# Kernel tuning notes

Hardware: AMD Instinct MI355X
Metric: run time of the kernel (lower is better)

Reference implementation:

```python
import jax, jax.numpy as jnp
import numpy as np

N = 50000      # nodes
E = 800000     # edges (before self-loops)
G = 128        # graphs in batch
IN = 128       # in_channels
HID = 32       # hidden_channels (per head)
HEADS = 4
OUT = 64       # out_channels
SLOPE = 0.2    # PyG GATConv default negative_slope


def setup_inputs() -> dict:
    key = jax.random.key(0)
    ks = jax.random.split(key, 24)
    s = 0.1
    inp = {
        'x': jax.random.normal(ks[0], (N, IN), jnp.float32),
        'edge_index': jax.random.randint(ks[1], (2, E), 0, N, dtype=jnp.int32),
        'batch': jnp.sort(jax.random.randint(ks[2], (N,), 0, G, dtype=jnp.int32)),
        # conv1: IN -> HEADS*HID, concat
        'W1': jax.random.normal(ks[3], (IN, HEADS * HID), jnp.float32) * s,
        'a1s': jax.random.normal(ks[4], (HEADS, HID), jnp.float32) * s,
        'a1d': jax.random.normal(ks[5], (HEADS, HID), jnp.float32) * s,
        'b1': jnp.zeros((HEADS * HID,), jnp.float32),
        # conv2: HEADS*HID -> HEADS*HID, concat
        'W2': jax.random.normal(ks[6], (HEADS * HID, HEADS * HID), jnp.float32) * s,
        'a2s': jax.random.normal(ks[7], (HEADS, HID), jnp.float32) * s,
        'a2d': jax.random.normal(ks[8], (HEADS, HID), jnp.float32) * s,
        'b2': jnp.zeros((HEADS * HID,), jnp.float32),
        # conv3
        'W3': jax.random.normal(ks[9], (HEADS * HID, HEADS * HID), jnp.float32) * s,
        'a3s': jax.random.normal(ks[10], (HEADS, HID), jnp.float32) * s,
        'a3d': jax.random.normal(ks[11], (HEADS, HID), jnp.float32) * s,
        'b3': jnp.zeros((HEADS * HID,), jnp.float32),
        # conv4: heads=1, concat=False -> HID
        'W4': jax.random.normal(ks[12], (HEADS * HID, 1 * HID), jnp.float32) * s,
        'a4s': jax.random.normal(ks[13], (1, HID), jnp.float32) * s,
        'a4d': jax.random.normal(ks[14], (1, HID), jnp.float32) * s,
        'b4': jnp.zeros((HID,), jnp.float32),
        # fc: HID -> OUT
        'fcW': jax.random.normal(ks[15], (HID, OUT), jnp.float32) * s,
        'fcb': jnp.zeros((OUT,), jnp.float32),
    }
    return inp


def gat_conv(x, src, dst, W, a_src, a_dst, bias, heads, ch, concat):
    # x: [N, F_in]; src/dst: [E'] with self-loops (PyG add_self_loops=True)
    h = (x @ W).reshape(N, heads, ch)                       # [N, H, C]
    alpha_s = jnp.einsum('nhc,hc->nh', h, a_src)            # [N, H]
    alpha_d = jnp.einsum('nhc,hc->nh', h, a_dst)
    e = jax.nn.leaky_relu(alpha_s[src] + alpha_d[dst], SLOPE)  # [E', H]
    # segment softmax over edges grouped by destination node
    e_max = jax.ops.segment_max(e, dst, num_segments=N)
    e = jnp.exp(e - e_max[dst])
    denom = jax.ops.segment_sum(e, dst, num_segments=N)
    alpha = e / (denom[dst] + 1e-16)                        # [E', H]
    msg = h[src] * alpha[:, :, None]                        # [E', H, C]
    out = jax.ops.segment_sum(msg, dst, num_segments=N)     # [N, H, C]
    out = out.reshape(N, heads * ch) if concat else out.mean(axis=1)
    return out + bias


def reference(x, edge_index, batch, W1, a1s, a1d, b1, W2, a2s, a2d, b2,
              W3, a3s, a3d, b3, W4, a4s, a4d, b4, fcW, fcb):
    loop = jnp.arange(N, dtype=edge_index.dtype)
    src = jnp.concatenate([edge_index[0], loop])            # add self-loops once
    dst = jnp.concatenate([edge_index[1], loop])
    h = jax.nn.elu(gat_conv(x, src, dst, W1, a1s, a1d, b1, HEADS, HID, True))
    h = jax.nn.elu(gat_conv(h, src, dst, W2, a2s, a2d, b2, HEADS, HID, True))
    h = jax.nn.elu(gat_conv(h, src, dst, W3, a3s, a3d, b3, HEADS, HID, True))
    h = jax.nn.elu(gat_conv(h, src, dst, W4, a4s, a4d, b4, 1, HID, False))
    # global mean pool over graphs
    counts = jax.ops.segment_sum(jnp.ones((N,), h.dtype), batch, num_segments=G)
    pooled = jax.ops.segment_sum(h, batch, num_segments=G) / jnp.maximum(counts, 1.0)[:, None]
    # dropout p=0.5 is identity at inference
    return pooled @ fcW + fcb                               # [G, OUT]
```

## Files before the change

kernel.cpp:

```cpp
#include <hip/hip_runtime.h>


constexpr int NN     = 50000;
constexpr int NNPAD  = 50048;
constexpr int EE     = 800000;
constexpr int ETOT   = EE + NN;
constexpr int GG     = 128;
constexpr int HIDC   = 32;
constexpr int OUTC   = 64;

constexpr int NRANGE = (NN + 127) / 128;
constexpr int EPB    = 4096;
constexpr int NBLK   = (EE + EPB - 1) / EPB;
constexpr int RCAP   = 2688;

typedef short  bf16x8 __attribute__((ext_vector_type(8)));
typedef float  f32x4  __attribute__((ext_vector_type(4)));

static __device__ __forceinline__ unsigned short f2bf(float f) {
    unsigned int u = __float_as_uint(f);
    unsigned int r = (u + 0x7fffu + ((u >> 16) & 1u)) >> 16;
    return (unsigned short)r;
}
static __device__ __forceinline__ float bflo(unsigned int v) {
    return __uint_as_float(v << 16);
}
static __device__ __forceinline__ float bfhi(unsigned int v) {
    return __uint_as_float(v & 0xffff0000u);
}

__global__ __launch_bounds__(256) void local_sort_kernel(
    const int* __restrict__ ei,
    unsigned int* __restrict__ blocksorted,
    int* __restrict__ boffs)
{
    __shared__ unsigned int sorted[EPB];
    __shared__ int hist[NRANGE + 1];
    __shared__ int scanv[NRANGE + 1];
    __shared__ int cur[NRANGE + 1];
    __shared__ int wsum4[4];
    __shared__ int ct_s;

    const int b = blockIdx.x, tid = threadIdx.x;
    const int lane = tid & 63, wid = tid >> 6;
    const int e0 = b * EPB;
    const int ecnt = min(EPB, EE - e0);

    for (int t = tid; t < NRANGE + 1; t += 256) hist[t] = 0;
    __syncthreads();

    unsigned int recs[16];
    int rkey[16];
#pragma unroll
    for (int k = 0; k < 16; ++k) {
        const int idx = tid + k * 256;
        rkey[k] = -1;
        if (idx < ecnt) {
            const int src = ei[e0 + idx];
            const int dst = ei[EE + e0 + idx];
            const int r = dst >> 7;
            recs[k] = (unsigned int)src | ((unsigned int)(dst & 127) << 16);
            rkey[k] = r;
            atomicAdd(&hist[r], 1);
        }
    }
    __syncthreads();

    int carry = 0;
    for (int base = 0; base < NRANGE + 1; base += 256) {
        const int i = base + tid;
        const int v = (i < NRANGE + 1) ? hist[i] : 0;
        int incl = v;
#pragma unroll
        for (int off = 1; off < 64; off <<= 1) {
            int t = __shfl_up(incl, off, 64);
            if (lane >= off) incl += t;
        }
        if (lane == 63) wsum4[wid] = incl;
        __syncthreads();
        if (tid == 0) {
            int s = 0;
#pragma unroll
            for (int w = 0; w < 4; ++w) { int t = wsum4[w]; wsum4[w] = s; s += t; }
            ct_s = s;
        }
        __syncthreads();
        const int excl = carry + wsum4[wid] + incl - v;
        if (i < NRANGE + 1) { scanv[i] = excl; cur[i] = excl; }
        carry += ct_s;
        __syncthreads();
    }

#pragma unroll
    for (int k = 0; k < 16; ++k) {
        if (rkey[k] >= 0) {
            const int pos = atomicAdd(&cur[rkey[k]], 1);
            sorted[pos] = recs[k];
        }
    }
    __syncthreads();

    for (int t = tid; t < ecnt; t += 256)
        blocksorted[(size_t)b * EPB + t] = sorted[t];
    for (int t = tid; t < NRANGE + 1; t += 256)
        boffs[b * (NRANGE + 1) + t] = scanv[t];
}

__global__ __launch_bounds__(512) void rbase_kernel(const int* __restrict__ boffs,
                                                    int* __restrict__ rbase)
{
    __shared__ int wsum[8], wpre[8];
    const int tid = threadIdx.x, lane = tid & 63, wid = tid >> 6;
    int tot = 0;
    if (tid < NRANGE) {
        for (int b = 0; b < NBLK; ++b) {
            const int* bp = boffs + b * (NRANGE + 1) + tid;
            tot += bp[1] - bp[0];
        }
        tot += min(128, NN - tid * 128);
    }
    int incl = tot;
#pragma unroll
    for (int off = 1; off < 64; off <<= 1) {
        int t = __shfl_up(incl, off, 64);
        if (lane >= off) incl += t;
    }
    if (lane == 63) wsum[wid] = incl;
    __syncthreads();
    if (tid < 8) {
        int wv = wsum[tid], winc = wv;
#pragma unroll
        for (int off = 1; off < 8; off <<= 1) {
            int t = __shfl_up(winc, off, 64);
            if (tid >= off) winc += t;
        }
        wpre[tid] = winc - wv;
    }
    __syncthreads();
    const int excl = wpre[wid] + incl - tot;
    if (tid < NRANGE) rbase[tid] = excl;
    if (tid == NRANGE - 1) rbase[NRANGE] = excl + tot;
}

__global__ __launch_bounds__(256) void phaseB_kernel(
    const int* __restrict__ boffs,
    const unsigned int* __restrict__ blocksorted,
    const int* __restrict__ rbase,
    int* __restrict__ offs,
    int* __restrict__ csrsrc)
{
    __shared__ unsigned int   rec[RCAP];
    __shared__ unsigned short outsrc[RCAP];
    __shared__ int runoff[NBLK + 1];
    __shared__ int bstart[NBLK];
    __shared__ int hist[128], lofs[128], cur[128];
    __shared__ int wsum4[4];
    __shared__ int tot0_s;

    const int r = blockIdx.x, tid = threadIdx.x;
    const int lane = tid & 63, wid = tid >> 6;
    const int base = r * 128;
    const int rn   = min(128, NN - base);

    int cnt = 0;
    if (tid < NBLK) {
        const int* bp = boffs + tid * (NRANGE + 1) + r;
        const int s = bp[0];
        bstart[tid] = s;
        cnt = bp[1] - s;
    }
    if (tid < 128) hist[tid] = 0;
    int incl = cnt;
#pragma unroll
    for (int off = 1; off < 64; off <<= 1) {
        int t = __shfl_up(incl, off, 64);
        if (lane >= off) incl += t;
    }
    if (lane == 63) wsum4[wid] = incl;
    __syncthreads();
    if (tid == 0) {
        int s = 0;
#pragma unroll
        for (int w = 0; w < 4; ++w) { int t = wsum4[w]; wsum4[w] = s; s += t; }
    }
    __syncthreads();
    const int excl = wsum4[wid] + incl - cnt;
    if (tid <= NBLK) runoff[tid] = excl;
    __syncthreads();

    const int tot8 = runoff[NBLK];
    for (int i = tid; i < tot8; i += 256) {
        int lo = 0, hi = NBLK;
        while (lo + 1 < hi) {
            const int mid = (lo + hi) >> 1;
            if (runoff[mid] <= i) lo = mid; else hi = mid;
        }
        rec[i] = blocksorted[(size_t)lo * EPB + bstart[lo] + (i - runoff[lo])];
    }
    for (int t = tid; t < rn; t += 256)
        rec[tot8 + t] = (unsigned int)(base + t) | ((unsigned int)t << 16);
    const int total = min(tot8 + rn, RCAP);
    __syncthreads();

    for (int t = tid; t < total; t += 256) atomicAdd(&hist[rec[t] >> 16], 1);
    __syncthreads();

    if (tid < 64) {
        int v = hist[tid], incl2 = v;
#pragma unroll
        for (int off = 1; off < 64; off <<= 1) {
            int t = __shfl_up(incl2, off, 64);
            if (tid >= off) incl2 += t;
        }
        lofs[tid] = incl2 - v;
        if (tid == 63) tot0_s = incl2;
    }
    __syncthreads();
    if (tid >= 64 && tid < 128) {
        const int l = tid & 63;
        int v = hist[tid], incl2 = v;
#pragma unroll
        for (int off = 1; off < 64; off <<= 1) {
            int t = __shfl_up(incl2, off, 64);
            if (l >= off) incl2 += t;
        }
        lofs[tid] = tot0_s + incl2 - v;
    }
    __syncthreads();

    if (tid < 128) cur[tid] = lofs[tid];
    if (tid < rn) offs[base + tid] = rbase[r] + lofs[tid];
    if (r == 0 && tid == 0) offs[NN] = rbase[NRANGE];
    __syncthreads();

    for (int t = tid; t < total; t += 256) {
        const unsigned int rc = rec[t];
        const int pos = atomicAdd(&cur[rc >> 16], 1);
        outsrc[pos] = (unsigned short)(rc & 0xffffu);
    }
    __syncthreads();
    const int rb = rbase[r];
    for (int t = tid; t < total; t += 256) csrsrc[rb + t] = (int)outsrc[t];
}

__global__ __launch_bounds__(256) void ahat_kernel(
    const float* __restrict__ W1, const float* __restrict__ a1s, const float* __restrict__ a1d,
    const float* __restrict__ W2, const float* __restrict__ a2s, const float* __restrict__ a2d,
    const float* __restrict__ W3, const float* __restrict__ a3s, const float* __restrict__ a3d,
    const float* __restrict__ W4, const float* __restrict__ a4s, const float* __restrict__ a4d,
    float* __restrict__ ahat)
{
    const int l = blockIdx.x;
    const float *W, *as_, *ad_;
    int fo, nh;
    if (l == 0)      { W = W1; as_ = a1s; ad_ = a1d; fo = 128; nh = 4; }
    else if (l == 1) { W = W2; as_ = a2s; ad_ = a2d; fo = 128; nh = 4; }
    else if (l == 2) { W = W3; as_ = a3s; ad_ = a3d; fo = 128; nh = 4; }
    else             { W = W4; as_ = a4s; ad_ = a4d; fo = 32;  nh = 1; }
    float* outp = ahat + l * 128 * 8;
    for (int item = threadIdx.x; item < 128 * 8; item += 256) {
        const int k = item >> 3, j = item & 7;
        const int hh = j & 3;
        const bool is_d = j >= 4;
        float v = 0.f;
        if (hh < nh) {
            const float* av = (is_d ? ad_ : as_) + hh * 32;
            const float* wp = W + (size_t)k * fo + hh * 32;
#pragma unroll 8
            for (int c = 0; c < 32; ++c) v = fmaf(wp[c], av[c], v);
        }
        outp[item] = v;
    }
}

__global__ void convert_x_kernel(const float* __restrict__ x, unsigned short* __restrict__ xb)
{
    int i = blockIdx.x * blockDim.x + threadIdx.x;
    if (i >= (NNPAD * 128) / 2) return;
    unsigned int packed = 0;
    if (2 * i < NN * 128) {
        float f0 = x[2 * i], f1 = x[2 * i + 1];
        packed = (unsigned int)f2bf(f0) | ((unsigned int)f2bf(f1) << 16);
    }
    reinterpret_cast<unsigned int*>(xb)[i] = packed;
}

template<int F_OUT, int NH>
__global__ __launch_bounds__(256) void gemm_mfma_kernel(
    const unsigned short* __restrict__ xb, const float* __restrict__ W,
    const float* __restrict__ ahat,
    unsigned short* __restrict__ hb,
    float* __restrict__ as_out, float* __restrict__ ad_out)
{
    constexpr int F_STG = F_OUT + 16;
    __shared__ unsigned short wt[F_STG * 128];
    const int tid = threadIdx.x;

    constexpr int PAIRS = F_STG * 64;
    for (int p = tid; p < PAIRS; p += 256) {
        const int n  = p % F_STG;
        const int k2 = p / F_STG;
        float w0 = 0.f, w1 = 0.f;
        if (n < F_OUT) {
            w0 = W[(size_t)(2 * k2) * F_OUT + n];
            w1 = W[(size_t)(2 * k2 + 1) * F_OUT + n];
        } else {
            const int j = n - F_OUT;
            if (j < 8) {
                w0 = ahat[(2 * k2) * 8 + j];
                w1 = ahat[(2 * k2 + 1) * 8 + j];
            }
        }
        const unsigned int packed = (unsigned int)f2bf(w0) | ((unsigned int)f2bf(w1) << 16);
        const int byte = n * 256 + ((4 * k2) ^ ((n & 7) << 4));
        *reinterpret_cast<unsigned int*>(reinterpret_cast<char*>(wt) + byte) = packed;
    }
    __syncthreads();

    const int wave = tid >> 6, lane = tid & 63;
    const int row0 = blockIdx.x * 64 + wave * 16;
    const int arow = row0 + (lane & 15);
    const int kchunk = (lane >> 4) * 8;

    const unsigned short* __restrict__ ap = xb + (size_t)arow * 128;
    bf16x8 a[4];
#pragma unroll
    for (int ks = 0; ks < 4; ++ks)
        a[ks] = *reinterpret_cast<const bf16x8*>(ap + ks * 32 + kchunk);

    const int kb_base = (lane >> 4) * 16;
    const int rbase = row0 + (lane >> 4) * 4;

#pragma unroll
    for (int nt = 0; nt < F_OUT / 16; ++nt) {
        const int n = nt * 16 + (lane & 15);
        f32x4 acc = {0.f, 0.f, 0.f, 0.f};
#pragma unroll
        for (int ks = 0; ks < 4; ++ks) {
            const int byte = n * 256 + ((ks * 64 + kb_base) ^ ((n & 7) << 4));
            bf16x8 b = *reinterpret_cast<const bf16x8*>(
                reinterpret_cast<const char*>(wt) + byte);
            acc = __builtin_amdgcn_mfma_f32_16x16x32_bf16(a[ks], b, acc, 0, 0, 0);
        }
#pragma unroll
        for (int r = 0; r < 4; ++r)
            hb[(size_t)(rbase + r) * F_OUT + n] = f2bf(acc[r]);
    }

    {
        const int n = F_OUT + (lane & 15);
        f32x4 acc = {0.f, 0.f, 0.f, 0.f};
#pragma unroll
        for (int ks = 0; ks < 4; ++ks) {
            const int byte = n * 256 + ((ks * 64 + kb_base) ^ ((n & 7) << 4));
            bf16x8 b = *reinterpret_cast<const bf16x8*>(
                reinterpret_cast<const char*>(wt) + byte);
            acc = __builtin_amdgcn_mfma_f32_16x16x32_bf16(a[ks], b, acc, 0, 0, 0);
        }
        const int col = lane & 15;
        if (col < 8) {
            const int hh = col & 3;
            const bool is_d = col >= 4;
            if (hh < NH) {
                float* op = is_d ? ad_out : as_out;
#pragma unroll
                for (int r = 0; r < 4; ++r) {
                    const int row = rbase + r;
                    if (row < NN) {
                        if (NH == 4) op[row * 4 + hh] = acc[r];
                        else         op[row]          = acc[r];
                    }
                }
            }
        }
    }
}

template<int HEADS, int F_OUT, bool OUT_BF16>
__global__ __launch_bounds__(64) void aggregate_kernel(
    const unsigned short* __restrict__ hlin,
    const float* __restrict__ as_,
    const float* __restrict__ ad_,
    const int* __restrict__ offs,
    const int* __restrict__ csr_src,
    const float* __restrict__ bias,
    void* __restrict__ out_v)
{
    const int d    = blockIdx.x;
    const int lane = threadIdx.x;
    const int beg  = offs[d], end = offs[d + 1];
    const int deg  = end - beg;

    float ad_h[HEADS];
#pragma unroll
    for (int h = 0; h < HEADS; ++h) ad_h[h] = ad_[d * HEADS + h];

    __shared__ float w_lds[64 * HEADS];
    __shared__ int   src_lds[64];

    float inv[HEADS];

    if (deg <= 64) {
        float ex[HEADS];
#pragma unroll
        for (int h = 0; h < HEADS; ++h) ex[h] = 0.f;
        int src = 0;
        if (lane < deg) {
            src = csr_src[beg + lane];
            if (HEADS == 4) {
                const float4 av = *reinterpret_cast<const float4*>(as_ + (size_t)src * 4);
                const float avv[4] = {av.x, av.y, av.z, av.w};
#pragma unroll
                for (int h = 0; h < 4; ++h) {
                    float e = avv[h] + ad_h[h];
                    e = fmaxf(e, 0.f) + 0.2f * fminf(e, 0.f);
                    ex[h] = __expf(e);
                }
            } else {
                float e = as_[src] + ad_h[0];
                e = fmaxf(e, 0.f) + 0.2f * fminf(e, 0.f);
                ex[0] = __expf(e);
            }
        }
        src_lds[lane] = src;
#pragma unroll
        for (int h = 0; h < HEADS; ++h) {
            float s = ex[h];
#pragma unroll
            for (int k = 1; k < 64; k <<= 1) s += __shfl_xor(s, k, 64);
            inv[h] = 1.f / (s + 1e-16f);
            w_lds[lane * HEADS + h] = ex[h] * inv[h];
        }
        __syncthreads();
    } else {
        float ssum[HEADS];
#pragma unroll
        for (int h = 0; h < HEADS; ++h) ssum[h] = 0.f;
        for (int p = beg + lane; p < end; p += 64) {
            const int src = csr_src[p];
            if (HEADS == 4) {
                const float4 av = *reinterpret_cast<const float4*>(as_ + (size_t)src * 4);
                const float avv[4] = {av.x, av.y, av.z, av.w};
#pragma unroll
                for (int h = 0; h < 4; ++h) {
                    float e = avv[h] + ad_h[h];
                    e = fmaxf(e, 0.f) + 0.2f * fminf(e, 0.f);
                    ssum[h] += __expf(e);
                }
            } else {
                float e = as_[src] + ad_h[0];
                e = fmaxf(e, 0.f) + 0.2f * fminf(e, 0.f);
                ssum[0] += __expf(e);
            }
        }
#pragma unroll
        for (int h = 0; h < HEADS; ++h) {
            float s = ssum[h];
#pragma unroll
            for (int k = 1; k < 64; k <<= 1) s += __shfl_xor(s, k, 64);
            inv[h] = 1.f / (s + 1e-16f);
        }
    }

    float acc[4] = {0.f, 0.f, 0.f, 0.f};

    for (int base = beg; base < end; base += 64) {
        const int cnt = min(64, end - base);
        if (deg > 64) {
            const int p = base + lane;
            int src = 0;
            float w[HEADS];
#pragma unroll
            for (int h = 0; h < HEADS; ++h) w[h] = 0.f;
            if (p < end) {
                src = csr_src[p];
                if (HEADS == 4) {
                    const float4 av = *reinterpret_cast<const float4*>(as_ + (size_t)src * 4);
                    const float avv[4] = {av.x, av.y, av.z, av.w};
#pragma unroll
                    for (int h = 0; h < 4; ++h) {
                        float e = avv[h] + ad_h[h];
                        e = fmaxf(e, 0.f) + 0.2f * fminf(e, 0.f);
                        w[h] = __expf(e) * inv[h];
                    }
                } else {
                    float e = as_[src] + ad_h[0];
                    e = fmaxf(e, 0.f) + 0.2f * fminf(e, 0.f);
                    w[0] = __expf(e) * inv[0];
                }
            }
            src_lds[lane] = src;
#pragma unroll
            for (int h = 0; h < HEADS; ++h) w_lds[lane * HEADS + h] = w[h];
            __syncthreads();
        }

        if (F_OUT == 128) {
            const int half = lane >> 5, cl = lane & 31;
            const int cntR = (cnt + 1) & ~1;
#pragma unroll 4
            for (int j = 0; j < cntR; j += 2) {
                const int   srcj = src_lds[j + half];
                const float w    = w_lds[(j + half) * 4 + (cl >> 3)];
                const uint2 hv   = *reinterpret_cast<const uint2*>(
                    hlin + (size_t)srcj * 128 + cl * 4);
                acc[0] = fmaf(w, bflo(hv.x), acc[0]);
                acc[1] = fmaf(w, bfhi(hv.x), acc[1]);
                acc[2] = fmaf(w, bflo(hv.y), acc[2]);
                acc[3] = fmaf(w, bfhi(hv.y), acc[3]);
            }
        } else {
            const int q = lane >> 4, cl = lane & 15;
            const int cntR = (cnt + 3) & ~3;
#pragma unroll 4
            for (int j = 0; j < cntR; j += 4) {
                const int   srcj = src_lds[j + q];
                const float w    = w_lds[j + q];
                const unsigned int hv = *reinterpret_cast<const unsigned int*>(
                    hlin + (size_t)srcj * 32 + cl * 2);
                acc[0] = fmaf(w, bflo(hv), acc[0]);
                acc[1] = fmaf(w, bfhi(hv), acc[1]);
            }
        }
        if (deg > 64) __syncthreads();
    }

    if (F_OUT == 128) {
#pragma unroll
        for (int t = 0; t < 4; ++t) acc[t] += __shfl_xor(acc[t], 32, 64);
        if (lane < 32) {
            const int c0 = lane * 4;
            float v[4];
#pragma unroll
            for (int t = 0; t < 4; ++t) {
                float v0 = acc[t] + bias[c0 + t];
                v[t] = (v0 > 0.f) ? v0 : (__expf(v0) - 1.f);
            }
            unsigned int p0 = (unsigned int)f2bf(v[0]) | ((unsigned int)f2bf(v[1]) << 16);
            unsigned int p1 = (unsigned int)f2bf(v[2]) | ((unsigned int)f2bf(v[3]) << 16);
            uint2* op = reinterpret_cast<uint2*>(
                (unsigned short*)out_v + (size_t)d * 128 + c0);
            *op = make_uint2(p0, p1);
        }
    } else {
        acc[0] += __shfl_xor(acc[0], 16, 64); acc[0] += __shfl_xor(acc[0], 32, 64);
        acc[1] += __shfl_xor(acc[1], 16, 64); acc[1] += __shfl_xor(acc[1], 32, 64);
        if (lane < 16) {
            const int c0 = lane * 2;
            float v0 = acc[0] + bias[c0];
            float v1 = acc[1] + bias[c0 + 1];
            v0 = (v0 > 0.f) ? v0 : (__expf(v0) - 1.f);
            v1 = (v1 > 0.f) ? v1 : (__expf(v1) - 1.f);
            if (OUT_BF16) {
                unsigned int pk = (unsigned int)f2bf(v0) | ((unsigned int)f2bf(v1) << 16);
                reinterpret_cast<unsigned int*>(out_v)[(size_t)d * 16 + lane] = pk;
            } else {
                reinterpret_cast<float2*>(out_v)[(size_t)d * 16 + lane] =
                    make_float2(v0, v1);
            }
        }
    }
}

__global__ __launch_bounds__(256) void pool_fc_kernel(
    const float* __restrict__ h4, const int* __restrict__ batch,
    const float* __restrict__ fcW, const float* __restrict__ fcb,
    float* __restrict__ out)
{
    const int g = blockIdx.x;
    __shared__ int sb, se;
    if (threadIdx.x == 0) {
        int lo = 0, hi = NN;
        while (lo < hi) { int mid = (lo + hi) >> 1; if (batch[mid] < g) lo = mid + 1; else hi = mid; }
        sb = lo;
        lo = sb; hi = NN;
        while (lo < hi) { int mid = (lo + hi) >> 1; if (batch[mid] < g + 1) lo = mid + 1; else hi = mid; }
        se = lo;
    }
    __syncthreads();
    const int s = sb, e = se;

    const int c  = threadIdx.x & 31;
    const int rg = threadIdx.x >> 5;
    float acc = 0.f;
    for (int n = s + rg; n < e; n += 8)
        acc += h4[(size_t)n * HIDC + c];

    __shared__ float red[8][32];
    red[rg][c] = acc;
    __syncthreads();
    __shared__ float pooled_s[32];
    if (threadIdx.x < 32) {
        float v = 0.f;
#pragma unroll
        for (int r = 0; r < 8; ++r) v += red[r][threadIdx.x];
        pooled_s[threadIdx.x] = v / fmaxf((float)(e - s), 1.f);
    }
    __syncthreads();
    if (threadIdx.x < OUTC) {
        const int o = threadIdx.x;
        float a2 = fcb[o];
#pragma unroll
        for (int cc = 0; cc < HIDC; ++cc)
            a2 = fmaf(pooled_s[cc], fcW[cc * OUTC + o], a2);
        out[g * OUTC + o] = a2;
    }
}

extern "C" void kernel_launch(void* const* d_in, const int* in_sizes, int n_in,
                              void* d_out, int out_size, void* d_ws, size_t ws_size,
                              hipStream_t stream)
{
    const float* x     = (const float*)d_in[0];
    const int*   ei    = (const int*)d_in[1];
    const int*   batch = (const int*)d_in[2];
    const float* W1  = (const float*)d_in[3];
    const float* a1s = (const float*)d_in[4];
    const float* a1d = (const float*)d_in[5];
    const float* b1  = (const float*)d_in[6];
    const float* W2  = (const float*)d_in[7];
    const float* a2s = (const float*)d_in[8];
    const float* a2d = (const float*)d_in[9];
    const float* b2  = (const float*)d_in[10];
    const float* W3  = (const float*)d_in[11];
    const float* a3s = (const float*)d_in[12];
    const float* a3d = (const float*)d_in[13];
    const float* b3  = (const float*)d_in[14];
    const float* W4  = (const float*)d_in[15];
    const float* a4s = (const float*)d_in[16];
    const float* a4d = (const float*)d_in[17];
    const float* b4  = (const float*)d_in[18];
    const float* fcW = (const float*)d_in[19];
    const float* fcb = (const float*)d_in[20];
    float* out = (float*)d_out;

    unsigned short* xb = (unsigned short*)d_ws;
    unsigned short* hb = xb + (size_t)NNPAD * 128;
    float* asb  = (float*)(hb + (size_t)NNPAD * 128);
    float* adb  = asb + (size_t)NN * 4;
    int*   offs   = (int*)(adb + (size_t)NN * 4);
    int*   csrsrc = offs + NN + 1;
    int*   boffs  = csrsrc + ETOT;
    int*   rbase  = boffs + NBLK * (NRANGE + 1);
    float* ahat   = (float*)(rbase + NRANGE + 1);
    unsigned int* blocksorted = (unsigned int*)hb;
    float* bufF = (float*)xb;

    local_sort_kernel<<<NBLK, 256, 0, stream>>>(ei, blocksorted, boffs);
    rbase_kernel<<<1, 512, 0, stream>>>(boffs, rbase);
    phaseB_kernel<<<NRANGE, 256, 0, stream>>>(boffs, blocksorted, rbase, offs, csrsrc);

    ahat_kernel<<<4, 256, 0, stream>>>(W1, a1s, a1d, W2, a2s, a2d,
                                       W3, a3s, a3d, W4, a4s, a4d, ahat);
    convert_x_kernel<<<(NNPAD * 64 + 255) / 256, 256, 0, stream>>>(x, xb);

    constexpr int GEMM_GRID = NNPAD / 64;

    gemm_mfma_kernel<128, 4><<<GEMM_GRID, 256, 0, stream>>>(xb, W1, ahat + 0 * 1024, hb, asb, adb);
    aggregate_kernel<4, 128, true><<<NN, 64, 0, stream>>>(hb, asb, adb, offs, csrsrc, b1, xb);
    gemm_mfma_kernel<128, 4><<<GEMM_GRID, 256, 0, stream>>>(xb, W2, ahat + 1 * 1024, hb, asb, adb);
    aggregate_kernel<4, 128, true><<<NN, 64, 0, stream>>>(hb, asb, adb, offs, csrsrc, b2, xb);
    gemm_mfma_kernel<128, 4><<<GEMM_GRID, 256, 0, stream>>>(xb, W3, ahat + 2 * 1024, hb, asb, adb);
    aggregate_kernel<4, 128, true><<<NN, 64, 0, stream>>>(hb, asb, adb, offs, csrsrc, b3, xb);
    gemm_mfma_kernel<32, 1><<<GEMM_GRID, 256, 0, stream>>>(xb, W4, ahat + 3 * 1024, hb, asb, adb);
    aggregate_kernel<1, 32, false><<<NN, 64, 0, stream>>>(hb, asb, adb, offs, csrsrc, b4, bufF);

    pool_fc_kernel<<<GG, 256, 0, stream>>>(bufF, batch, fcW, fcb, out);
}
```

Measured before the change: 293.2 us.

## Precompute swizzled bf16 weights once and pack four nodes per aggregate block

The weight transpose, bf16 conversion and attention-vector folding move from every GEMM block into a one-time prep kernel. Each GEMM block then only performs a vectorized copy into LDS. The aggregation kernel now processes four destination nodes per 256-thread block, one per wave, and replaces block barriers with LDS wait counters. The aim is to cut redundant per-block weight work and per-block scheduling overhead, at the cost of a larger workspace and relying on wave-local LDS ordering.

```diff
diff --git a/kernel.cpp b/kernel.cpp
--- a/kernel.cpp
+++ b/kernel.cpp
@@ -243,22 +243,24 @@
     for (int t = tid; t < total; t += 256) csrsrc[rb + t] = (int)outsrc[t];
 }
 
-__global__ __launch_bounds__(256) void ahat_kernel(
+__global__ __launch_bounds__(256) void prep_kernel(
     const float* __restrict__ W1, const float* __restrict__ a1s, const float* __restrict__ a1d,
     const float* __restrict__ W2, const float* __restrict__ a2s, const float* __restrict__ a2d,
     const float* __restrict__ W3, const float* __restrict__ a3s, const float* __restrict__ a3d,
     const float* __restrict__ W4, const float* __restrict__ a4s, const float* __restrict__ a4d,
-    float* __restrict__ ahat)
-{
-    const int l = blockIdx.x;
+    unsigned short* __restrict__ wtg)
+{
+    __shared__ float ahat_s[128 * 8];
+    const int l = blockIdx.x, tid = threadIdx.x;
     const float *W, *as_, *ad_;
     int fo, nh;
     if (l == 0)      { W = W1; as_ = a1s; ad_ = a1d; fo = 128; nh = 4; }
     else if (l == 1) { W = W2; as_ = a2s; ad_ = a2d; fo = 128; nh = 4; }
     else if (l == 2) { W = W3; as_ = a3s; ad_ = a3d; fo = 128; nh = 4; }
     else             { W = W4; as_ = a4s; ad_ = a4d; fo = 32;  nh = 1; }
-    float* outp = ahat + l * 128 * 8;
-    for (int item = threadIdx.x; item < 128 * 8; item += 256) {
+    const int F_STG = fo + 16;
+
+    for (int item = tid; item < 128 * 8; item += 256) {
         const int k = item >> 3, j = item & 7;
         const int hh = j & 3;
         const bool is_d = j >= 4;
@@ -269,7 +271,28 @@
 #pragma unroll 8
             for (int c = 0; c < 32; ++c) v = fmaf(wp[c], av[c], v);
         }
-        outp[item] = v;
+        ahat_s[item] = v;
+    }
+    __syncthreads();
+
+    unsigned short* outb = wtg + (size_t)l * (144 * 128);
+    for (int p = tid; p < F_STG * 64; p += 256) {
+        const int n  = p % F_STG;
+        const int k2 = p / F_STG;
+        float w0 = 0.f, w1 = 0.f;
+        if (n < fo) {
+            w0 = W[(size_t)(2 * k2) * fo + n];
+            w1 = W[(size_t)(2 * k2 + 1) * fo + n];
+        } else {
+            const int j = n - fo;
+            if (j < 8) {
+                w0 = ahat_s[(2 * k2) * 8 + j];
+                w1 = ahat_s[(2 * k2 + 1) * 8 + j];
+            }
+        }
+        const unsigned int packed = (unsigned int)f2bf(w0) | ((unsigned int)f2bf(w1) << 16);
+        const int byte = n * 256 + ((4 * k2) ^ ((n & 7) << 4));
+        *reinterpret_cast<unsigned int*>(reinterpret_cast<char*>(outb) + byte) = packed;
     }
 }
 
@@ -287,8 +310,8 @@
 
 template<int F_OUT, int NH>
 __global__ __launch_bounds__(256) void gemm_mfma_kernel(
-    const unsigned short* __restrict__ xb, const float* __restrict__ W,
-    const float* __restrict__ ahat,
+    const unsigned short* __restrict__ xb,
+    const unsigned short* __restrict__ wtg,
     unsigned short* __restrict__ hb,
     float* __restrict__ as_out, float* __restrict__ ad_out)
 {
@@ -296,24 +319,13 @@
     __shared__ unsigned short wt[F_STG * 128];
     const int tid = threadIdx.x;
 
-    constexpr int PAIRS = F_STG * 64;
-    for (int p = tid; p < PAIRS; p += 256) {
-        const int n  = p % F_STG;
-        const int k2 = p / F_STG;
-        float w0 = 0.f, w1 = 0.f;
-        if (n < F_OUT) {
-            w0 = W[(size_t)(2 * k2) * F_OUT + n];
-            w1 = W[(size_t)(2 * k2 + 1) * F_OUT + n];
-        } else {
-            const int j = n - F_OUT;
-            if (j < 8) {
-                w0 = ahat[(2 * k2) * 8 + j];
-                w1 = ahat[(2 * k2 + 1) * 8 + j];
-            }
-        }
-        const unsigned int packed = (unsigned int)f2bf(w0) | ((unsigned int)f2bf(w1) << 16);
-        const int byte = n * 256 + ((4 * k2) ^ ((n & 7) << 4));
-        *reinterpret_cast<unsigned int*>(reinterpret_cast<char*>(wt) + byte) = packed;
+    {
+        const bf16x8* __restrict__ wg = reinterpret_cast<const bf16x8*>(wtg);
+        bf16x8* wl = reinterpret_cast<bf16x8*>(wt);
+        constexpr int NV = F_STG * 16;
+#pragma unroll
+        for (int i = 0; i < NV / 256; ++i)
+            wl[i * 256 + tid] = wg[i * 256 + tid];
     }
     __syncthreads();
 
@@ -377,7 +389,7 @@
 }
 
 template<int HEADS, int F_OUT, bool OUT_BF16>
-__global__ __launch_bounds__(64) void aggregate_kernel(
+__global__ __launch_bounds__(256) void aggregate_kernel(
     const unsigned short* __restrict__ hlin,
     const float* __restrict__ as_,
     const float* __restrict__ ad_,
@@ -386,17 +398,21 @@
     const float* __restrict__ bias,
     void* __restrict__ out_v)
 {
-    const int d    = blockIdx.x;
-    const int lane = threadIdx.x;
+    __shared__ float w_all[4][64 * HEADS];
+    __shared__ int   s_all[4][64];
+    const int wave = threadIdx.x >> 6;
+    const int lane = threadIdx.x & 63;
+    const int d    = blockIdx.x * 4 + wave;
+    if (d >= NN) return;
+    float* __restrict__ w_lds  = w_all[wave];
+    int*   __restrict__ src_lds = s_all[wave];
+
     const int beg  = offs[d], end = offs[d + 1];
     const int deg  = end - beg;
 
     float ad_h[HEADS];
 #pragma unroll
     for (int h = 0; h < HEADS; ++h) ad_h[h] = ad_[d * HEADS + h];
-
-    __shared__ float w_lds[64 * HEADS];
-    __shared__ int   src_lds[64];
 
     float inv[HEADS];
 
@@ -431,7 +447,7 @@
             inv[h] = 1.f / (s + 1e-16f);
             w_lds[lane * HEADS + h] = ex[h] * inv[h];
         }
-        __syncthreads();
+        asm volatile("s_waitcnt lgkmcnt(0)" ::: "memory");
     } else {
         float ssum[HEADS];
 #pragma unroll
@@ -492,7 +508,7 @@
             src_lds[lane] = src;
 #pragma unroll
             for (int h = 0; h < HEADS; ++h) w_lds[lane * HEADS + h] = w[h];
-            __syncthreads();
+            asm volatile("s_waitcnt lgkmcnt(0)" ::: "memory");
         }
 
         if (F_OUT == 128) {
@@ -522,7 +538,6 @@
                 acc[1] = fmaf(w, bfhi(hv), acc[1]);
             }
         }
-        if (deg > 64) __syncthreads();
     }
 
     if (F_OUT == 128) {
@@ -642,7 +657,7 @@
     int*   csrsrc = offs + NN + 1;
     int*   boffs  = csrsrc + ETOT;
     int*   rbase  = boffs + NBLK * (NRANGE + 1);
-    float* ahat   = (float*)(rbase + NRANGE + 1);
+    unsigned short* wtg = (unsigned short*)(rbase + NRANGE + 1);
     unsigned int* blocksorted = (unsigned int*)hb;
     float* bufF = (float*)xb;
 
@@ -650,20 +665,22 @@
     rbase_kernel<<<1, 512, 0, stream>>>(boffs, rbase);
     phaseB_kernel<<<NRANGE, 256, 0, stream>>>(boffs, blocksorted, rbase, offs, csrsrc);
 
-    ahat_kernel<<<4, 256, 0, stream>>>(W1, a1s, a1d, W2, a2s, a2d,
-                                       W3, a3s, a3d, W4, a4s, a4d, ahat);
+    prep_kernel<<<4, 256, 0, stream>>>(W1, a1s, a1d, W2, a2s, a2d,
+                                       W3, a3s, a3d, W4, a4s, a4d, wtg);
     convert_x_kernel<<<(NNPAD * 64 + 255) / 256, 256, 0, stream>>>(x, xb);
 
     constexpr int GEMM_GRID = NNPAD / 64;
-
-    gemm_mfma_kernel<128, 4><<<GEMM_GRID, 256, 0, stream>>>(xb, W1, ahat + 0 * 1024, hb, asb, adb);
-    aggregate_kernel<4, 128, true><<<NN, 64, 0, stream>>>(hb, asb, adb, offs, csrsrc, b1, xb);
-    gemm_mfma_kernel<128, 4><<<GEMM_GRID, 256, 0, stream>>>(xb, W2, ahat + 1 * 1024, hb, asb, adb);
-    aggregate_kernel<4, 128, true><<<NN, 64, 0, stream>>>(hb, asb, adb, offs, csrsrc, b2, xb);
-    gemm_mfma_kernel<128, 4><<<GEMM_GRID, 256, 0, stream>>>(xb, W3, ahat + 2 * 1024, hb, asb, adb);
-    aggregate_kernel<4, 128, true><<<NN, 64, 0, stream>>>(hb, asb, adb, offs, csrsrc, b3, xb);
-    gemm_mfma_kernel<32, 1><<<GEMM_GRID, 256, 0, stream>>>(xb, W4, ahat + 3 * 1024, hb, asb, adb);
-    aggregate_kernel<1, 32, false><<<NN, 64, 0, stream>>>(hb, asb, adb, offs, csrsrc, b4, bufF);
+    constexpr int AGG_GRID  = (NN + 3) / 4;
+    constexpr size_t WSTRIDE = 144 * 128;
+
+    gemm_mfma_kernel<128, 4><<<GEMM_GRID, 256, 0, stream>>>(xb, wtg + 0 * WSTRIDE, hb, asb, adb);
+    aggregate_kernel<4, 128, true><<<AGG_GRID, 256, 0, stream>>>(hb, asb, adb, offs, csrsrc, b1, xb);
+    gemm_mfma_kernel<128, 4><<<GEMM_GRID, 256, 0, stream>>>(xb, wtg + 1 * WSTRIDE, hb, asb, adb);
+    aggregate_kernel<4, 128, true><<<AGG_GRID, 256, 0, stream>>>(hb, asb, adb, offs, csrsrc, b2, xb);
+    gemm_mfma_kernel<128, 4><<<GEMM_GRID, 256, 0, stream>>>(xb, wtg + 2 * WSTRIDE, hb, asb, adb);
+    aggregate_kernel<4, 128, true><<<AGG_GRID, 256, 0, stream>>>(hb, asb, adb, offs, csrsrc, b3, xb);
+    gemm_mfma_kernel<32, 1><<<GEMM_GRID, 256, 0, stream>>>(xb, wtg + 3 * WSTRIDE, hb, asb, adb);
+    aggregate_kernel<1, 32, false><<<AGG_GRID, 256, 0, stream>>>(hb, asb, adb, offs, csrsrc, b4, bufF);
 
     pool_fc_kernel<<<GG, 256, 0, stream>>>(bufF, batch, fcW, fcb, out);
 }
```

Result: faster. 266.4 us (-9.2%).
